# Kernel tuning notes

Hardware: AMD Instinct MI355X
Metric: run time of the kernel (lower is better)

Reference implementation:

```python
import jax, jax.numpy as jnp
import numpy as np

H = 256   # hidden_dim
K = 4     # number of z_layer Linears
T = 8192  # number of permutation trees (Z-nodes) in the batch
C = 16    # children (leaf indices) per tree
N = 200000  # rows in batch.x node-feature table


def setup_inputs() -> dict:
    key = jax.random.key(0)
    ks = jax.random.split(key, 6)
    x = jax.random.normal(ks[0], (N, H), dtype=jnp.float32)
    leaf_idx = jax.random.randint(ks[1], (T, C), 0, N)
    # z_layer: k Linears (y = x @ W + b), z_final_layer: one Linear
    scale = 1.0 / np.sqrt(H)
    Wz = jax.random.uniform(ks[2], (K, H, H), dtype=jnp.float32, minval=-scale, maxval=scale)
    bz = jax.random.uniform(ks[3], (K, H), dtype=jnp.float32, minval=-scale, maxval=scale)
    Wzf = jax.random.uniform(ks[4], (H, H), dtype=jnp.float32, minval=-scale, maxval=scale)
    bzf = jax.random.uniform(ks[5], (H,), dtype=jnp.float32, minval=-scale, maxval=scale)
    return {"x": x, "Wz": Wz, "bz": bz, "Wzf": Wzf, "bzf": bzf, "leaf_idx": leaf_idx}


def reference(x, Wz, bz, Wzf, bzf, leaf_idx):
    # Batched z_layer_fn over T trees, each a Z-node over C leaf children.
    data = x[leaf_idx]                                   # [T, C, H] gather (fetch_or_produce)
    # k parallel Linears: [K, T, C, H]
    after = jnp.einsum('tch,khd->ktcd', data, Wz) + bz[:, None, None, :]
    # embedding_k[torch.roll(arange(C), shifts=k)] == roll(embedding_k, k, axis=children)
    k = after.shape[0]
    rolled_sum = after[0]
    for i in range(1, k):  # tiny fixed loop over k layers
        rolled_sum = rolled_sum + jnp.roll(after[i], i, axis=1)
    h = jax.nn.elu(rolled_sum)                           # [T, C, H]
    h = jnp.einsum('tch,hd->tcd', h, Wzf) + bzf          # z_final_layer
    out = jax.nn.elu(jnp.sum(h, axis=1))                 # sum over children, ELU -> [T, H]
    return out
```

## Files before the change

kernel.cpp:

```cpp
#include <hip/hip_runtime.h>
#include <stdint.h>

#define TREES 8192
#define HID   256
#define CH    16
#define KL    4
#define G     4
#define LDSS  264

typedef short bf16x8 __attribute__((ext_vector_type(8)));
typedef float f32x4  __attribute__((ext_vector_type(4)));

__device__ __forceinline__ unsigned short f2bf(float f) {
    unsigned u = __builtin_bit_cast(unsigned, f);
    u += 0x7FFFu + ((u >> 16) & 1u);
    return (unsigned short)(u >> 16);
}
__device__ __forceinline__ float elu1(float x) {
    return x > 0.f ? x : (__expf(x) - 1.f);
}
__device__ __forceinline__ uint4 pack8(float4 a, float4 b) {
    union { uint4 u4; unsigned short s[8]; } U;
    U.s[0] = f2bf(a.x); U.s[1] = f2bf(a.y); U.s[2] = f2bf(a.z); U.s[3] = f2bf(a.w);
    U.s[4] = f2bf(b.x); U.s[5] = f2bf(b.y); U.s[6] = f2bf(b.z); U.s[7] = f2bf(b.w);
    return U.u4;
}

__global__ void prep_transpose(const float* __restrict__ Wz,
                               const float* __restrict__ Wzf,
                               const float* __restrict__ bz,
                               unsigned short* __restrict__ WzT,
                               unsigned short* __restrict__ WzfT,
                               float* __restrict__ bzsum) {
    __shared__ unsigned short ts[64][65];
    const int k  = blockIdx.z;
    const int h0 = blockIdx.x * 64;
    const int d0 = blockIdx.y * 64;
    const float* src = (k < KL) ? (Wz + (k << 16)) : Wzf;
    unsigned short* dst = (k < KL) ? (WzT + (k << 16)) : WzfT;
    const int tid = threadIdx.x;
    const int jc  = tid & 63;
    #pragma unroll
    for (int r = 0; r < 16; ++r) {
        int i = r * 4 + (tid >> 6);
        ts[jc][i] = f2bf(src[(h0 + i) * HID + d0 + jc]);
    }
    __syncthreads();
    #pragma unroll
    for (int r = 0; r < 16; ++r) {
        int jl = r * 4 + (tid >> 6);
        dst[(d0 + jl) * HID + h0 + jc] = ts[jl][jc];
    }
    if (k == KL && blockIdx.x == 0 && blockIdx.y == 0) {
        float s = 0.f;
        #pragma unroll
        for (int kk = 0; kk < KL; ++kk) s += bz[kk * HID + tid];
        bzsum[tid] = s;
    }
}

__global__ __launch_bounds__(256, 3) void ptree_kernel(
    const float* __restrict__ x,
    const int* __restrict__ leaf,
    const float* __restrict__ bzf,
    const unsigned short* __restrict__ WzT,
    const unsigned short* __restrict__ WzfT,
    const float* __restrict__ bzsum,
    float* __restrict__ out,
    int nrows)
{
    __shared__ __align__(16) unsigned short sh[G][CH][LDSS];
    __shared__ __align__(16) unsigned short hs[G][LDSS];
    const int tid  = threadIdx.x;
    const int lane = tid & 63;
    const int wave = tid >> 6;
    const int t0   = blockIdx.x * G;
    const int ncol = lane & 15;
    const int quad = lane >> 4;

    #pragma unroll
    for (int i = 0; i < (G * CH * 32) / 256; ++i) {
        int cid = i * 256 + tid;
        int g   = cid >> 9;
        int row = (cid >> 5) & 15;
        int ch  = cid & 31;
        int idx = leaf[(t0 + g) * CH + row];
        idx = ((unsigned)idx < (unsigned)nrows) ? idx : 0;
        const float* src = x + (size_t)idx * HID + ch * 8;
        float4 v0 = *(const float4*)src;
        float4 v1 = *(const float4*)(src + 4);
        *(uint4*)&sh[g][row][ch * 8] = pack8(v0, v1);
    }

    float bzs[4], bzfv[4];
    #pragma unroll
    for (int nt = 0; nt < 4; ++nt) {
        bzs[nt]  = bzsum[wave * 64 + nt * 16 + ncol];
        bzfv[nt] = bzf[wave * 64 + nt * 16 + ncol];
    }

    __syncthreads();

    f32x4 acc1[G][4];
    #pragma unroll
    for (int g = 0; g < G; ++g)
        #pragma unroll
        for (int nt = 0; nt < 4; ++nt) acc1[g][nt] = f32x4{0.f, 0.f, 0.f, 0.f};

    const unsigned short* wz_base = WzT + (wave * 64 + ncol) * HID + quad * 8;

    #pragma unroll 4
    for (int s = 0; s < KL * 8; ++s) {
        const int k  = s >> 3;
        const int kt = s & 7;
        const unsigned short* bp = wz_base + k * 65536 + kt * 32;
        bf16x8 b[4];
        #pragma unroll
        for (int nt = 0; nt < 4; ++nt)
            b[nt] = *(const bf16x8*)(bp + nt * 16 * HID);
        const int arow = (ncol - k) & 15;
        #pragma unroll
        for (int g = 0; g < G; ++g) {
            bf16x8 a = *(const bf16x8*)&sh[g][arow][kt * 32 + quad * 8];
            #pragma unroll
            for (int nt = 0; nt < 4; ++nt)
                acc1[g][nt] = __builtin_amdgcn_mfma_f32_16x16x32_bf16(
                    a, b[nt], acc1[g][nt], 0, 0, 0);
        }
    }

    #pragma unroll
    for (int g = 0; g < G; ++g)
        #pragma unroll
        for (int nt = 0; nt < 4; ++nt) {
            float sv = 0.f;
            #pragma unroll
            for (int r = 0; r < 4; ++r) sv += elu1(acc1[g][nt][r] + bzs[nt]);
            sv += __shfl_xor(sv, 16);
            sv += __shfl_xor(sv, 32);
            if (quad == 0) hs[g][wave * 64 + nt * 16 + ncol] = f2bf(sv);
        }

    __syncthreads();

    f32x4 acc2[4];
    #pragma unroll
    for (int nt = 0; nt < 4; ++nt) acc2[nt] = f32x4{0.f, 0.f, 0.f, 0.f};

    const unsigned short* wzf_base = WzfT + (wave * 64 + ncol) * HID + quad * 8;
    #pragma unroll
    for (int kt = 0; kt < 8; ++kt) {
        bf16x8 a = *(const bf16x8*)&hs[ncol & (G - 1)][kt * 32 + quad * 8];
        if (ncol >= G) a = bf16x8{0, 0, 0, 0, 0, 0, 0, 0};
        #pragma unroll
        for (int nt = 0; nt < 4; ++nt) {
            bf16x8 b = *(const bf16x8*)(wzf_base + nt * 16 * HID + kt * 32);
            acc2[nt] = __builtin_amdgcn_mfma_f32_16x16x32_bf16(a, b, acc2[nt], 0, 0, 0);
        }
    }

    #pragma unroll
    for (int nt = 0; nt < 4; ++nt)
        #pragma unroll
        for (int r = 0; r < 4; ++r) {
            int tree = quad * 4 + r;
            if (tree < G) {
                float v = elu1(acc2[nt][r] + 16.f * bzfv[nt]);
                out[(size_t)(t0 + tree) * HID + wave * 64 + nt * 16 + ncol] = v;
            }
        }
}

extern "C" void kernel_launch(void* const* d_in, const int* in_sizes, int n_in,
                              void* d_out, int out_size, void* d_ws, size_t ws_size,
                              hipStream_t stream) {
    (void)out_size; (void)ws_size;
    const void* p_x = nullptr; const void* p_Wz = nullptr; const void* p_bz = nullptr;
    const void* p_Wzf = nullptr; const void* p_bzf = nullptr; const void* p_leaf = nullptr;
    for (int i = 0; i < n_in; ++i) {
        switch (in_sizes[i]) {
            case 200000 * 256:   p_x    = d_in[i]; break;
            case KL * 256 * 256: p_Wz   = d_in[i]; break;
            case KL * 256:       p_bz   = d_in[i]; break;
            case 256 * 256:      p_Wzf  = d_in[i]; break;
            case 256:            p_bzf  = d_in[i]; break;
            case TREES * CH:     p_leaf = d_in[i]; break;
        }
    }
    const float* x    = (const float*)p_x;
    const float* Wz   = (const float*)p_Wz;
    const float* bz   = (const float*)p_bz;
    const float* Wzf  = (const float*)p_Wzf;
    const float* bzf  = (const float*)p_bzf;
    const int*   leaf = (const int*)p_leaf;

    unsigned short* WzT  = (unsigned short*)d_ws;
    unsigned short* WzfT = WzT + KL * HID * HID;
    float*          bzsum = (float*)(WzfT + HID * HID);

    dim3 tg(4, 4, KL + 1);
    prep_transpose<<<tg, 256, 0, stream>>>(Wz, Wzf, bz, WzT, WzfT, bzsum);
    ptree_kernel<<<TREES / G, 256, 0, stream>>>(x, leaf, bzf, WzT, WzfT, bzsum,
                                                (float*)d_out, 200000);
}
```

Before: 407.7 us.

## Stage Wz fragments into double-buffered LDS via async global-to-LDS loads

Each step's Wz weight slice is no longer read straight from global memory into registers. It is prefetched one step ahead into a double-buffered LDS region with global_load_lds, and every MFMA step ends in a block barrier. The gathered activation tile now uses an XOR-swizzled layout in place of padding, to avoid LDS bank conflicts. The aim is to hide weight-load latency behind MFMA work. The price is more LDS per block, lower launch-bounds occupancy (3 to 2) and 32 extra barriers per block.

```diff
diff --git a/kernel.cpp b/kernel.cpp
--- a/kernel.cpp
+++ b/kernel.cpp
@@ -6,7 +6,7 @@
 #define CH    16
 #define KL    4
 #define G     4
-#define LDSS  264
+#define NSTEP (KL * 8)
 
 typedef short bf16x8 __attribute__((ext_vector_type(8)));
 typedef float f32x4  __attribute__((ext_vector_type(4)));
@@ -24,6 +24,11 @@
     U.s[0] = f2bf(a.x); U.s[1] = f2bf(a.y); U.s[2] = f2bf(a.z); U.s[3] = f2bf(a.w);
     U.s[4] = f2bf(b.x); U.s[5] = f2bf(b.y); U.s[6] = f2bf(b.z); U.s[7] = f2bf(b.w);
     return U.u4;
+}
+__device__ __forceinline__ void gload_lds16(const void* g, void* l) {
+    __builtin_amdgcn_global_load_lds(
+        (const __attribute__((address_space(1))) void*)g,
+        (__attribute__((address_space(3))) void*)l, 16, 0, 0);
 }
 
 __global__ void prep_transpose(const float* __restrict__ Wz,
@@ -59,7 +64,7 @@
     }
 }
 
-__global__ __launch_bounds__(256, 3) void ptree_kernel(
+__global__ __launch_bounds__(256, 2) void ptree_kernel(
     const float* __restrict__ x,
     const int* __restrict__ leaf,
     const float* __restrict__ bzf,
@@ -69,8 +74,9 @@
     float* __restrict__ out,
     int nrows)
 {
-    __shared__ __align__(16) unsigned short sh[G][CH][LDSS];
-    __shared__ __align__(16) unsigned short hs[G][LDSS];
+    __shared__ __align__(16) unsigned short shA[G * CH * 256];
+    __shared__ __align__(16) unsigned short shB[2][8192];
+    __shared__ __align__(16) unsigned short hs[G][264];
     const int tid  = threadIdx.x;
     const int lane = tid & 63;
     const int wave = tid >> 6;
@@ -78,8 +84,17 @@
     const int ncol = lane & 15;
     const int quad = lane >> 4;
 
-    #pragma unroll
-    for (int i = 0; i < (G * CH * 32) / 256; ++i) {
+    const int dd   = tid >> 2;
+    const int q    = tid & 3;
+    const int srcq = q ^ ((dd >> 1) & 3);
+    const unsigned short* gstage = WzT + dd * HID + srcq * 8;
+
+    #pragma unroll
+    for (int c = 0; c < 4; ++c)
+        gload_lds16(gstage + c * 16384, &shB[0][c * 2048 + tid * 8]);
+
+    #pragma unroll
+    for (int i = 0; i < 8; ++i) {
         int cid = i * 256 + tid;
         int g   = cid >> 9;
         int row = (cid >> 5) & 15;
@@ -89,7 +104,7 @@
         const float* src = x + (size_t)idx * HID + ch * 8;
         float4 v0 = *(const float4*)src;
         float4 v1 = *(const float4*)(src + 4);
-        *(uint4*)&sh[g][row][ch * 8] = pack8(v0, v1);
+        *(uint4*)&shA[(g * CH + row) * 256 + ((ch ^ (row & 7)) * 8)] = pack8(v0, v1);
     }
 
     float bzs[4], bzfv[4];
@@ -99,6 +114,13 @@
         bzfv[nt] = bzf[wave * 64 + nt * 16 + ncol];
     }
 
+    int boff[4];
+    #pragma unroll
+    for (int nt = 0; nt < 4; ++nt) {
+        const int d = wave * 64 + nt * 16 + ncol;
+        boff[nt] = d * 32 + ((quad ^ ((d >> 1) & 3)) * 8);
+    }
+
     __syncthreads();
 
     f32x4 acc1[G][4];
@@ -107,26 +129,33 @@
         #pragma unroll
         for (int nt = 0; nt < 4; ++nt) acc1[g][nt] = f32x4{0.f, 0.f, 0.f, 0.f};
 
-    const unsigned short* wz_base = WzT + (wave * 64 + ncol) * HID + quad * 8;
-
-    #pragma unroll 4
-    for (int s = 0; s < KL * 8; ++s) {
+    #pragma unroll 2
+    for (int s = 0; s < NSTEP; ++s) {
         const int k  = s >> 3;
         const int kt = s & 7;
-        const unsigned short* bp = wz_base + k * 65536 + kt * 32;
-        bf16x8 b[4];
+        if (s < NSTEP - 1) {
+            const int sn = s + 1;
+            const unsigned short* gsrc = gstage + (sn >> 3) * 65536 + (sn & 7) * 32;
+            unsigned short* ldst = &shB[sn & 1][tid * 8];
+            #pragma unroll
+            for (int c = 0; c < 4; ++c)
+                gload_lds16(gsrc + c * 16384, ldst + c * 2048);
+        }
+        bf16x8 bfr[4];
         #pragma unroll
         for (int nt = 0; nt < 4; ++nt)
-            b[nt] = *(const bf16x8*)(bp + nt * 16 * HID);
-        const int arow = (ncol - k) & 15;
+            bfr[nt] = *(const bf16x8*)&shB[s & 1][boff[nt]];
+        const int arow  = (ncol - k) & 15;
+        const int abase = arow * 256 + (((kt * 4 + quad) ^ (arow & 7)) * 8);
         #pragma unroll
         for (int g = 0; g < G; ++g) {
-            bf16x8 a = *(const bf16x8*)&sh[g][arow][kt * 32 + quad * 8];
+            bf16x8 a = *(const bf16x8*)&shA[g * (CH * 256) + abase];
             #pragma unroll
             for (int nt = 0; nt < 4; ++nt)
                 acc1[g][nt] = __builtin_amdgcn_mfma_f32_16x16x32_bf16(
-                    a, b[nt], acc1[g][nt], 0, 0, 0);
-        }
+                    a, bfr[nt], acc1[g][nt], 0, 0, 0);
+        }
+        __syncthreads();
     }
 
     #pragma unroll
```

New measurement: 378.0 us. 7.3% less time.

## Process 16 trees per block in two groups and prefetch weight fragments

Applied to the files above, without the earlier changes.

Each block now handles 16 trees in two sequential groups of 8 instead of 4 trees. Doubling the trees per pass reuses each weight fragment load across more MFMAs, and the second GEMM fills all 16 MFMA rows rather than padding 12 with zeros. Weight fragments for the next step are prefetched into registers while the current step's MFMAs run. The cost is higher register and LDS use (launch bounds drop to 2 blocks per SM) and serialised gathers between groups, which lowers occupancy and the latency hiding for the random row gathers.

```diff
diff --git a/kernel.cpp b/kernel.cpp
--- a/kernel.cpp
+++ b/kernel.cpp
@@ -5,7 +5,9 @@
 #define HID   256
 #define CH    16
 #define KL    4
-#define G     4
+#define G     8
+#define NG    2
+#define GB    (G * NG)
 #define LDSS  264
 
 typedef short bf16x8 __attribute__((ext_vector_type(8)));
@@ -59,7 +61,7 @@
     }
 }
 
-__global__ __launch_bounds__(256, 3) void ptree_kernel(
+__global__ __launch_bounds__(256, 2) void ptree_kernel(
     const float* __restrict__ x,
     const int* __restrict__ leaf,
     const float* __restrict__ bzf,
@@ -70,27 +72,13 @@
     int nrows)
 {
     __shared__ __align__(16) unsigned short sh[G][CH][LDSS];
-    __shared__ __align__(16) unsigned short hs[G][LDSS];
+    __shared__ __align__(16) unsigned short hs[GB][LDSS];
     const int tid  = threadIdx.x;
     const int lane = tid & 63;
     const int wave = tid >> 6;
-    const int t0   = blockIdx.x * G;
+    const int t0   = blockIdx.x * GB;
     const int ncol = lane & 15;
     const int quad = lane >> 4;
-
-    #pragma unroll
-    for (int i = 0; i < (G * CH * 32) / 256; ++i) {
-        int cid = i * 256 + tid;
-        int g   = cid >> 9;
-        int row = (cid >> 5) & 15;
-        int ch  = cid & 31;
-        int idx = leaf[(t0 + g) * CH + row];
-        idx = ((unsigned)idx < (unsigned)nrows) ? idx : 0;
-        const float* src = x + (size_t)idx * HID + ch * 8;
-        float4 v0 = *(const float4*)src;
-        float4 v1 = *(const float4*)(src + 4);
-        *(uint4*)&sh[g][row][ch * 8] = pack8(v0, v1);
-    }
 
     float bzs[4], bzfv[4];
     #pragma unroll
@@ -99,59 +87,83 @@
         bzfv[nt] = bzf[wave * 64 + nt * 16 + ncol];
     }
 
-    __syncthreads();
-
-    f32x4 acc1[G][4];
-    #pragma unroll
-    for (int g = 0; g < G; ++g)
-        #pragma unroll
-        for (int nt = 0; nt < 4; ++nt) acc1[g][nt] = f32x4{0.f, 0.f, 0.f, 0.f};
-
     const unsigned short* wz_base = WzT + (wave * 64 + ncol) * HID + quad * 8;
 
-    #pragma unroll 4
-    for (int s = 0; s < KL * 8; ++s) {
-        const int k  = s >> 3;
-        const int kt = s & 7;
-        const unsigned short* bp = wz_base + k * 65536 + kt * 32;
-        bf16x8 b[4];
+    for (int grp = 0; grp < NG; ++grp) {
+        const int tg = t0 + grp * G;
+
+        #pragma unroll
+        for (int i = 0; i < (G * CH * 32) / 256; ++i) {
+            int cid = i * 256 + tid;
+            int g   = cid >> 9;
+            int row = (cid >> 5) & 15;
+            int ch  = cid & 31;
+            int idx = leaf[(tg + g) * CH + row];
+            idx = ((unsigned)idx < (unsigned)nrows) ? idx : 0;
+            const float* src = x + (size_t)idx * HID + ch * 8;
+            float4 v0 = *(const float4*)src;
+            float4 v1 = *(const float4*)(src + 4);
+            *(uint4*)&sh[g][row][ch * 8] = pack8(v0, v1);
+        }
+
+        __syncthreads();
+
+        f32x4 acc1[G][4];
+        #pragma unroll
+        for (int g = 0; g < G; ++g)
+            #pragma unroll
+            for (int nt = 0; nt < 4; ++nt) acc1[g][nt] = f32x4{0.f, 0.f, 0.f, 0.f};
+
+        bf16x8 bc[4], bn[4];
         #pragma unroll
         for (int nt = 0; nt < 4; ++nt)
-            b[nt] = *(const bf16x8*)(bp + nt * 16 * HID);
-        const int arow = (ncol - k) & 15;
-        #pragma unroll
-        for (int g = 0; g < G; ++g) {
-            bf16x8 a = *(const bf16x8*)&sh[g][arow][kt * 32 + quad * 8];
+            bc[nt] = *(const bf16x8*)(wz_base + nt * 16 * HID);
+
+        #pragma unroll 2
+        for (int s = 0; s < KL * 8; ++s) {
+            const int sn = (s < KL * 8 - 1) ? s + 1 : s;
+            const unsigned short* pn = wz_base + (sn >> 3) * 65536 + (sn & 7) * 32;
             #pragma unroll
             for (int nt = 0; nt < 4; ++nt)
-                acc1[g][nt] = __builtin_amdgcn_mfma_f32_16x16x32_bf16(
-                    a, b[nt], acc1[g][nt], 0, 0, 0);
-        }
-    }
-
-    #pragma unroll
-    for (int g = 0; g < G; ++g)
-        #pragma unroll
-        for (int nt = 0; nt < 4; ++nt) {
-            float sv = 0.f;
-            #pragma unroll
-            for (int r = 0; r < 4; ++r) sv += elu1(acc1[g][nt][r] + bzs[nt]);
-            sv += __shfl_xor(sv, 16);
-            sv += __shfl_xor(sv, 32);
-            if (quad == 0) hs[g][wave * 64 + nt * 16 + ncol] = f2bf(sv);
-        }
-
-    __syncthreads();
+                bn[nt] = *(const bf16x8*)(pn + nt * 16 * HID);
+            const int k    = s >> 3;
+            const int kt   = s & 7;
+            const int arow = (ncol - k) & 15;
+            #pragma unroll
+            for (int g = 0; g < G; ++g) {
+                bf16x8 a = *(const bf16x8*)&sh[g][arow][kt * 32 + quad * 8];
+                #pragma unroll
+                for (int nt = 0; nt < 4; ++nt)
+                    acc1[g][nt] = __builtin_amdgcn_mfma_f32_16x16x32_bf16(
+                        a, bc[nt], acc1[g][nt], 0, 0, 0);
+            }
+            #pragma unroll
+            for (int nt = 0; nt < 4; ++nt) bc[nt] = bn[nt];
+        }
+
+        #pragma unroll
+        for (int g = 0; g < G; ++g)
+            #pragma unroll
+            for (int nt = 0; nt < 4; ++nt) {
+                float sv = 0.f;
+                #pragma unroll
+                for (int r = 0; r < 4; ++r) sv += elu1(acc1[g][nt][r] + bzs[nt]);
+                sv += __shfl_xor(sv, 16);
+                sv += __shfl_xor(sv, 32);
+                if (quad == 0) hs[grp * G + g][wave * 64 + nt * 16 + ncol] = f2bf(sv);
+            }
+
+        __syncthreads();
+    }
 
     f32x4 acc2[4];
     #pragma unroll
     for (int nt = 0; nt < 4; ++nt) acc2[nt] = f32x4{0.f, 0.f, 0.f, 0.f};
 
     const unsigned short* wzf_base = WzfT + (wave * 64 + ncol) * HID + quad * 8;
-    #pragma unroll
+    #pragma unroll 2
     for (int kt = 0; kt < 8; ++kt) {
-        bf16x8 a = *(const bf16x8*)&hs[ncol & (G - 1)][kt * 32 + quad * 8];
-        if (ncol >= G) a = bf16x8{0, 0, 0, 0, 0, 0, 0, 0};
+        bf16x8 a = *(const bf16x8*)&hs[ncol][kt * 32 + quad * 8];
         #pragma unroll
         for (int nt = 0; nt < 4; ++nt) {
             bf16x8 b = *(const bf16x8*)(wzf_base + nt * 16 * HID + kt * 32);
@@ -163,11 +175,9 @@
     for (int nt = 0; nt < 4; ++nt)
         #pragma unroll
         for (int r = 0; r < 4; ++r) {
-            int tree = quad * 4 + r;
-            if (tree < G) {
-                float v = elu1(acc2[nt][r] + 16.f * bzfv[nt]);
-                out[(size_t)(t0 + tree) * HID + wave * 64 + nt * 16 + ncol] = v;
-            }
+            const int tree = quad * 4 + r;
+            float v = elu1(acc2[nt][r] + 16.f * bzfv[nt]);
+            out[(size_t)(t0 + tree) * HID + wave * 64 + nt * 16 + ncol] = v;
         }
 }
 
@@ -200,6 +210,6 @@
 
     dim3 tg(4, 4, KL + 1);
     prep_transpose<<<tg, 256, 0, stream>>>(Wz, Wzf, bz, WzT, WzfT, bzsum);
-    ptree_kernel<<<TREES / G, 256, 0, stream>>>(x, leaf, bzf, WzT, WzfT, bzsum,
-                                                (float*)d_out, 200000);
-}
+    ptree_kernel<<<TREES / GB, 256, 0, stream>>>(x, leaf, bzf, WzT, WzfT, bzsum,
+                                                 (float*)d_out, 200000);
+}
```

Result: faster. 342.1 us (-16.1%).
